# Kernel tuning notes

Measured on AMD Instinct MI355X. Metric: run time of the kernel, lower is better.

## Reference

```python
import jax, jax.numpy as jnp
import numpy as np

N = 1_000_000          # number of query points
POINT_DIMS = 2         # (x, y) coordinates
NUM_EMB = 6572         # number of video frames
EMB_DIM = 32
HIDDEN = 128


def setup_inputs() -> dict:
    key = jax.random.key(0)
    ks = jax.random.split(key, 10)
    x = jax.random.uniform(ks[0], (N, POINT_DIMS), dtype=jnp.float32)
    # fractional frame index in [0, NUM_EMB - 1)
    embeddings = jax.random.uniform(ks[1], (N,), dtype=jnp.float32) * (NUM_EMB - 1)
    em_table = jax.random.normal(ks[2], (NUM_EMB, EMB_DIM), dtype=jnp.float32) * 0.1
    in0 = POINT_DIMS + EMB_DIM
    W0 = jax.random.normal(ks[3], (in0, HIDDEN), dtype=jnp.float32) / np.sqrt(in0)
    b0 = jax.random.normal(ks[4], (HIDDEN,), dtype=jnp.float32) * 0.01
    W1 = jax.random.normal(ks[5], (HIDDEN, HIDDEN), dtype=jnp.float32) / np.sqrt(HIDDEN)
    b1 = jax.random.normal(ks[6], (HIDDEN,), dtype=jnp.float32) * 0.01
    W2 = jax.random.normal(ks[7], (HIDDEN, 1), dtype=jnp.float32) / np.sqrt(HIDDEN)
    b2 = jax.random.normal(ks[8], (1,), dtype=jnp.float32) * 0.01
    return {"x": x, "embeddings": embeddings, "em_table": em_table,
            "W0": W0, "b0": b0, "W1": W1, "b1": b1, "W2": W2, "b2": b2}


def reference(x, embeddings, em_table, W0, b0, W1, b1, W2, b2):
    num_emb = em_table.shape[0]
    em1 = embeddings.astype(jnp.int32)                       # floor (inputs >= 0)
    em2 = jnp.minimum(em1 + 1, num_emb - 1)                  # clamp(em1+1, max=E-1)
    res = (embeddings - em1.astype(jnp.float32))[:, None]    # [N, 1]
    e1 = em_table[em1]                                       # [N, 32] gather
    e2 = em_table[em2]                                       # [N, 32] gather
    em = e1 + (e2 - e1) * res                                # lerp
    h = jnp.concatenate((x, em), axis=1) @ W0 + b0           # [N, 128]
    h = jnp.clip(h, 0.0, 1.0)
    h = jnp.clip(h @ W1 + b1, 0.0, 1.0)
    out = jax.nn.sigmoid(h @ W2 + b2)                        # [N, 1]
    return out
```

## Files before the change

### kernel.cpp

```cpp
#include <hip/hip_runtime.h>
#include <hip/hip_bf16.h>


using bf16x8 = __attribute__((ext_vector_type(8))) short;
using f32x4  = __attribute__((ext_vector_type(4))) float;

#define NPTS    1000000
#define NUMEMB  6572
#define HID     128
#define M_IT    64
#define A0S     72
#define H0S     136
#define TILES   (NPTS / M_IT)
#define NBLOCKS 768

__device__ __forceinline__ unsigned short bf16r(float f) {
    unsigned u;
    __builtin_memcpy(&u, &f, 4);
    u = (u + 0x7fffu + ((u >> 16) & 1u)) >> 16;
    return (unsigned short)u;
}
__device__ __forceinline__ unsigned pk2(float a, float b) {
    float2 f2; f2.x = a; f2.y = b;
    __hip_bfloat162 h = __float22bfloat162_rn(f2);
    unsigned u;
    __builtin_memcpy(&u, &h, 4);
    return u;
}
__device__ __forceinline__ float clamp01(float x) {
    return __builtin_amdgcn_fmed3f(x, 0.f, 1.f);
}

__global__ __launch_bounds__(256, 3)
void mlp_fused(const float* __restrict__ x,
               const float* __restrict__ emb,
               const float* __restrict__ em_table,
               const float* __restrict__ W0, const float* __restrict__ b0,
               const float* __restrict__ W1, const float* __restrict__ b1,
               const float* __restrict__ W2, const float* __restrict__ b2,
               float* __restrict__ out)
{
    __shared__ __align__(16) unsigned short A0[2 * M_IT * A0S];
    __shared__ __align__(16) unsigned short H0[M_IT * H0S];
    __shared__ __align__(16) float PART[16][65];

    const int tid  = threadIdx.x;
    const int lane = tid & 63;
    const int nq   = tid >> 6;
    const int q    = lane >> 4;
    const int cl   = lane & 15;
    const int p    = tid >> 2;
    const int s    = tid & 3;

    for (int i = tid; i < 2 * M_IT * A0S; i += 256) A0[i] = 0;

    const int hcol = nq * 32 + (cl >> 2) * 8 + (cl & 3);
    bf16x8 w0t[2][2];
    for (int hb = 0; hb < 2; ++hb)
        for (int kt = 0; kt < 2; ++kt) {
            const int col = hcol + hb * 4;
            bf16x8 v;
            #pragma unroll
            for (int e = 0; e < 8; ++e) {
                const int k = kt * 32 + q * 8 + e;
                float val = 0.f;
                if (k < 32)       val = W0[(2 + k) * HID + col];
                else if (k == 32) val = W0[0 * HID + col];
                else if (k == 33) val = W0[1 * HID + col];
                v[e] = (short)bf16r(val);
            }
            w0t[hb][kt] = v;
        }

    bf16x8 w1r[2][4];
    for (int hb = 0; hb < 2; ++hb)
        for (int kk = 0; kk < 4; ++kk) {
            const int kt  = (nq + kk) & 3;
            const int col = hcol + hb * 4;
            bf16x8 v;
            #pragma unroll
            for (int e = 0; e < 8; ++e) {
                const int k = kt * 32 + q * 8 + e;
                v[e] = (short)bf16r(W1[k * HID + col]);
            }
            w1r[hb][kk] = v;
        }

    f32x4 b0q[2], b1q[2], w2q[2];
    for (int hb = 0; hb < 2; ++hb)
        for (int r = 0; r < 4; ++r) {
            const int h = nq * 32 + q * 8 + hb * 4 + r;
            b0q[hb][r] = b0[h];
            b1q[hb][r] = b1[h];
            w2q[hb][r] = W2[h];
        }
    const float bias2 = b2[0];

    int t = blockIdx.x;
    int cur = 0;
    {
        const int gp = t * M_IT + p;
        const float fe = emb[gp];
        float2 xv = {0.f, 0.f};
        if (s == 0) xv = *(const float2*)(x + 2 * gp);
        const int e1 = (int)fe;
        const int e2 = (e1 + 1 < NUMEMB) ? e1 + 1 : NUMEMB - 1;
        const float r = fe - (float)e1;
        const float4* p1 = (const float4*)(em_table + e1 * 32 + s * 8);
        const float4* p2 = (const float4*)(em_table + e2 * 32 + s * 8);
        const float4 g0 = p1[0], g1 = p1[1], g2 = p2[0], g3 = p2[1];
        uint4 d;
        d.x = pk2(g0.x + (g2.x - g0.x) * r, g0.y + (g2.y - g0.y) * r);
        d.y = pk2(g0.z + (g2.z - g0.z) * r, g0.w + (g2.w - g0.w) * r);
        d.z = pk2(g1.x + (g3.x - g1.x) * r, g1.y + (g3.y - g1.y) * r);
        d.w = pk2(g1.z + (g3.z - g1.z) * r, g1.w + (g3.w - g1.w) * r);
        *(uint4*)&A0[p * A0S + s * 8] = d;
        if (s == 0) *(unsigned*)&A0[p * A0S + 32] = pk2(xv.x, xv.y);
    }
    float  feB;
    float2 xvB = {0.f, 0.f};
    {
        int t1 = t + gridDim.x; if (t1 >= TILES) t1 = t;
        const int gp = t1 * M_IT + p;
        feB = emb[gp];
        if (s == 0) xvB = *(const float2*)(x + 2 * gp);
    }

    __syncthreads();

    for (; t < TILES; t += gridDim.x, cur ^= 1) {
        const int base = t * M_IT;
        const unsigned short* A0c = A0 + cur * (M_IT * A0S);
        unsigned short*       A0n = A0 + (cur ^ 1) * (M_IT * A0S);

        f32x4 acc[4][2];
        #pragma unroll
        for (int pb = 0; pb < 4; ++pb)
            #pragma unroll
            for (int hb = 0; hb < 2; ++hb)
                acc[pb][hb] = b0q[hb];
        #pragma unroll
        for (int pb = 0; pb < 4; ++pb) {
            #pragma unroll
            for (int kt = 0; kt < 2; ++kt) {
                bf16x8 bfrag = *(const bf16x8*)
                    &A0c[(pb * 16 + cl) * A0S + kt * 32 + q * 8];
                #pragma unroll
                for (int hb = 0; hb < 2; ++hb)
                    acc[pb][hb] = __builtin_amdgcn_mfma_f32_16x16x32_bf16(
                        w0t[hb][kt], bfrag, acc[pb][hb], 0, 0, 0);
            }
        }

        const int ge1 = (int)feB;
        const int ge2 = (ge1 + 1 < NUMEMB) ? ge1 + 1 : NUMEMB - 1;
        const float4* gp1 = (const float4*)(em_table + ge1 * 32 + s * 8);
        const float4* gp2 = (const float4*)(em_table + ge2 * 32 + s * 8);
        const float4 g0 = gp1[0], g1 = gp1[1], g2 = gp2[0], g3 = gp2[1];

        uint4 own[4];
        #pragma unroll
        for (int pb = 0; pb < 4; ++pb) {
            const f32x4 v0 = acc[pb][0], v1 = acc[pb][1];
            uint4 w;
            w.x = pk2(clamp01(v0[0]), clamp01(v0[1]));
            w.y = pk2(clamp01(v0[2]), clamp01(v0[3]));
            w.z = pk2(clamp01(v1[0]), clamp01(v1[1]));
            w.w = pk2(clamp01(v1[2]), clamp01(v1[3]));
            own[pb] = w;
            *(uint4*)&H0[(pb * 16 + cl) * H0S + nq * 32 + q * 8] = w;
        }

        {
            const float r = feB - (float)ge1;
            uint4 d;
            d.x = pk2(g0.x + (g2.x - g0.x) * r, g0.y + (g2.y - g0.y) * r);
            d.y = pk2(g0.z + (g2.z - g0.z) * r, g0.w + (g2.w - g0.w) * r);
            d.z = pk2(g1.x + (g3.x - g1.x) * r, g1.y + (g3.y - g1.y) * r);
            d.w = pk2(g1.z + (g3.z - g1.z) * r, g1.w + (g3.w - g1.w) * r);
            *(uint4*)&A0n[p * A0S + s * 8] = d;
            if (s == 0) *(unsigned*)&A0n[p * A0S + 32] = pk2(xvB.x, xvB.y);
        }
        {
            int t2 = t + 2 * (int)gridDim.x; if (t2 >= TILES) t2 = t;
            const int gp = t2 * M_IT + p;
            feB = emb[gp];
            if (s == 0) xvB = *(const float2*)(x + 2 * gp);
        }
        __syncthreads();

        #pragma unroll
        for (int pb = 0; pb < 4; ++pb)
            #pragma unroll
            for (int hb = 0; hb < 2; ++hb)
                acc[pb][hb] = b1q[hb];
        #pragma unroll
        for (int pb = 0; pb < 4; ++pb) {
            bf16x8 bfrag;
            __builtin_memcpy(&bfrag, &own[pb], 16);
            #pragma unroll
            for (int hb = 0; hb < 2; ++hb)
                acc[pb][hb] = __builtin_amdgcn_mfma_f32_16x16x32_bf16(
                    w1r[hb][0], bfrag, acc[pb][hb], 0, 0, 0);
        }
        #pragma unroll
        for (int kk = 1; kk < 4; ++kk) {
            const int kcol = (((nq + kk) & 3) << 5) + q * 8;
            #pragma unroll
            for (int pb = 0; pb < 4; ++pb) {
                bf16x8 bfrag = *(const bf16x8*)
                    &H0[(pb * 16 + cl) * H0S + kcol];
                #pragma unroll
                for (int hb = 0; hb < 2; ++hb)
                    acc[pb][hb] = __builtin_amdgcn_mfma_f32_16x16x32_bf16(
                        w1r[hb][kk], bfrag, acc[pb][hb], 0, 0, 0);
            }
        }

        #pragma unroll
        for (int pb = 0; pb < 4; ++pb) {
            float sum = 0.f;
            #pragma unroll
            for (int hb = 0; hb < 2; ++hb) {
                const f32x4 v = acc[pb][hb];
                sum += clamp01(v[0]) * w2q[hb][0];
                sum += clamp01(v[1]) * w2q[hb][1];
                sum += clamp01(v[2]) * w2q[hb][2];
                sum += clamp01(v[3]) * w2q[hb][3];
            }
            PART[nq * 4 + q][pb * 16 + cl] = sum;
        }
        __syncthreads();

        if (tid < 64) {
            float z = bias2;
            #pragma unroll
            for (int i = 0; i < 16; ++i) z += PART[i][tid];
            out[base + tid] = 1.f / (1.f + __expf(-z));
        }
    }
}

extern "C" void kernel_launch(void* const* d_in, const int* in_sizes, int n_in,
                              void* d_out, int out_size, void* d_ws, size_t ws_size,
                              hipStream_t stream) {
    const float* x   = (const float*)d_in[0];
    const float* emb = (const float*)d_in[1];
    const float* emt = (const float*)d_in[2];
    const float* W0  = (const float*)d_in[3];
    const float* b0  = (const float*)d_in[4];
    const float* W1  = (const float*)d_in[5];
    const float* b1  = (const float*)d_in[6];
    const float* W2  = (const float*)d_in[7];
    const float* b2  = (const float*)d_in[8];
    mlp_fused<<<NBLOCKS, 256, 0, stream>>>(x, emb, emt, W0, b0, W1, b1, W2, b2,
                                           (float*)d_out);
}
```

Before: 126.5 us.

## Split MFMA work 2x2 across waves to cut LDS reads of hidden layer

Each wave now owns 64 hidden columns for 32 points instead of 32 columns for all 64 points. Two of the four K-slices of layer 1 then come from the wave's own registers rather than LDS, which halves the H0 reads and the partial-sum reduction. The cost is twice the weight-fragment registers per wave. To fit them, launch bounds drop to 2 blocks per CU and the grid shrinks to 512 blocks, which lowers occupancy and latency hiding for the embedding gathers.

```diff
diff --git a/kernel.cpp b/kernel.cpp
--- a/kernel.cpp
+++ b/kernel.cpp
@@ -12,7 +12,7 @@
 #define A0S     72
 #define H0S     136
 #define TILES   (NPTS / M_IT)
-#define NBLOCKS 768
+#define NBLOCKS 512
 
 __device__ __forceinline__ unsigned short bf16r(float f) {
     unsigned u;
@@ -31,7 +31,7 @@
     return __builtin_amdgcn_fmed3f(x, 0.f, 1.f);
 }
 
-__global__ __launch_bounds__(256, 3)
+__global__ __launch_bounds__(256, 2)
 void mlp_fused(const float* __restrict__ x,
                const float* __restrict__ emb,
                const float* __restrict__ em_table,
@@ -42,23 +42,26 @@
 {
     __shared__ __align__(16) unsigned short A0[2 * M_IT * A0S];
     __shared__ __align__(16) unsigned short H0[M_IT * H0S];
-    __shared__ __align__(16) float PART[16][65];
+    __shared__ __align__(16) float PART2[8][65];
 
     const int tid  = threadIdx.x;
     const int lane = tid & 63;
-    const int nq   = tid >> 6;
+    const int w    = tid >> 6;
+    const int h2   = w & 1;
+    const int p2   = w >> 1;
     const int q    = lane >> 4;
     const int cl   = lane & 15;
     const int p    = tid >> 2;
     const int s    = tid & 3;
+    const int pbase = p2 * 32;
 
     for (int i = tid; i < 2 * M_IT * A0S; i += 256) A0[i] = 0;
 
-    const int hcol = nq * 32 + (cl >> 2) * 8 + (cl & 3);
-    bf16x8 w0t[2][2];
-    for (int hb = 0; hb < 2; ++hb)
+    const int mrow = (cl >> 2) * 8 + (cl & 3);
+    bf16x8 w0t[4][2];
+    for (int hb = 0; hb < 4; ++hb)
         for (int kt = 0; kt < 2; ++kt) {
-            const int col = hcol + hb * 4;
+            const int col = h2 * 64 + (hb >> 1) * 32 + mrow + (hb & 1) * 4;
             bf16x8 v;
             #pragma unroll
             for (int e = 0; e < 8; ++e) {
@@ -72,24 +75,24 @@
             w0t[hb][kt] = v;
         }
 
-    bf16x8 w1r[2][4];
-    for (int hb = 0; hb < 2; ++hb)
+    bf16x8 w1r[4][4];
+    for (int hb = 0; hb < 4; ++hb)
         for (int kk = 0; kk < 4; ++kk) {
-            const int kt  = (nq + kk) & 3;
-            const int col = hcol + hb * 4;
+            const int ktg = (h2 * 2 + kk) & 3;
+            const int col = h2 * 64 + (hb >> 1) * 32 + mrow + (hb & 1) * 4;
             bf16x8 v;
             #pragma unroll
             for (int e = 0; e < 8; ++e) {
-                const int k = kt * 32 + q * 8 + e;
+                const int k = ktg * 32 + q * 8 + e;
                 v[e] = (short)bf16r(W1[k * HID + col]);
             }
             w1r[hb][kk] = v;
         }
 
-    f32x4 b0q[2], b1q[2], w2q[2];
-    for (int hb = 0; hb < 2; ++hb)
+    f32x4 b0q[4], b1q[4], w2q[4];
+    for (int hb = 0; hb < 4; ++hb)
         for (int r = 0; r < 4; ++r) {
-            const int h = nq * 32 + q * 8 + hb * 4 + r;
+            const int h = h2 * 64 + (hb >> 1) * 32 + q * 8 + (hb & 1) * 4 + r;
             b0q[hb][r] = b0[h];
             b1q[hb][r] = b1[h];
             w2q[hb][r] = W2[h];
@@ -107,8 +110,8 @@
         const int e2 = (e1 + 1 < NUMEMB) ? e1 + 1 : NUMEMB - 1;
         const float r = fe - (float)e1;
         const float4* p1 = (const float4*)(em_table + e1 * 32 + s * 8);
-        const float4* p2 = (const float4*)(em_table + e2 * 32 + s * 8);
-        const float4 g0 = p1[0], g1 = p1[1], g2 = p2[0], g3 = p2[1];
+        const float4* p2p = (const float4*)(em_table + e2 * 32 + s * 8);
+        const float4 g0 = p1[0], g1 = p1[1], g2 = p2p[0], g3 = p2p[1];
         uint4 d;
         d.x = pk2(g0.x + (g2.x - g0.x) * r, g0.y + (g2.y - g0.y) * r);
         d.y = pk2(g0.z + (g2.z - g0.z) * r, g0.w + (g2.w - g0.w) * r);
@@ -133,20 +136,20 @@
         const unsigned short* A0c = A0 + cur * (M_IT * A0S);
         unsigned short*       A0n = A0 + (cur ^ 1) * (M_IT * A0S);
 
-        f32x4 acc[4][2];
-        #pragma unroll
-        for (int pb = 0; pb < 4; ++pb)
-            #pragma unroll
-            for (int hb = 0; hb < 2; ++hb)
+        f32x4 acc[2][4];
+        #pragma unroll
+        for (int pb = 0; pb < 2; ++pb)
+            #pragma unroll
+            for (int hb = 0; hb < 4; ++hb)
                 acc[pb][hb] = b0q[hb];
         #pragma unroll
-        for (int pb = 0; pb < 4; ++pb) {
+        for (int pb = 0; pb < 2; ++pb) {
             #pragma unroll
             for (int kt = 0; kt < 2; ++kt) {
                 bf16x8 bfrag = *(const bf16x8*)
-                    &A0c[(pb * 16 + cl) * A0S + kt * 32 + q * 8];
+                    &A0c[(pbase + pb * 16 + cl) * A0S + kt * 32 + q * 8];
                 #pragma unroll
-                for (int hb = 0; hb < 2; ++hb)
+                for (int hb = 0; hb < 4; ++hb)
                     acc[pb][hb] = __builtin_amdgcn_mfma_f32_16x16x32_bf16(
                         w0t[hb][kt], bfrag, acc[pb][hb], 0, 0, 0);
             }
@@ -158,18 +161,22 @@
         const float4* gp2 = (const float4*)(em_table + ge2 * 32 + s * 8);
         const float4 g0 = gp1[0], g1 = gp1[1], g2 = gp2[0], g3 = gp2[1];
 
-        uint4 own[4];
-        #pragma unroll
-        for (int pb = 0; pb < 4; ++pb) {
-            const f32x4 v0 = acc[pb][0], v1 = acc[pb][1];
-            uint4 w;
-            w.x = pk2(clamp01(v0[0]), clamp01(v0[1]));
-            w.y = pk2(clamp01(v0[2]), clamp01(v0[3]));
-            w.z = pk2(clamp01(v1[0]), clamp01(v1[1]));
-            w.w = pk2(clamp01(v1[2]), clamp01(v1[3]));
-            own[pb] = w;
-            *(uint4*)&H0[(pb * 16 + cl) * H0S + nq * 32 + q * 8] = w;
-        }
+        uint4 own[2][2];
+        #pragma unroll
+        for (int pb = 0; pb < 2; ++pb)
+            #pragma unroll
+            for (int ktl = 0; ktl < 2; ++ktl) {
+                const f32x4 v0 = acc[pb][2 * ktl + 0];
+                const f32x4 v1 = acc[pb][2 * ktl + 1];
+                uint4 wv;
+                wv.x = pk2(clamp01(v0[0]), clamp01(v0[1]));
+                wv.y = pk2(clamp01(v0[2]), clamp01(v0[3]));
+                wv.z = pk2(clamp01(v1[0]), clamp01(v1[1]));
+                wv.w = pk2(clamp01(v1[2]), clamp01(v1[3]));
+                own[pb][ktl] = wv;
+                *(uint4*)&H0[(pbase + pb * 16 + cl) * H0S
+                             + h2 * 64 + ktl * 32 + q * 8] = wv;
+            }
 
         {
             const float r = feB - (float)ge1;
@@ -190,52 +197,55 @@
         __syncthreads();
 
         #pragma unroll
-        for (int pb = 0; pb < 4; ++pb)
-            #pragma unroll
-            for (int hb = 0; hb < 2; ++hb)
+        for (int pb = 0; pb < 2; ++pb)
+            #pragma unroll
+            for (int hb = 0; hb < 4; ++hb)
                 acc[pb][hb] = b1q[hb];
         #pragma unroll
-        for (int pb = 0; pb < 4; ++pb) {
-            bf16x8 bfrag;
-            __builtin_memcpy(&bfrag, &own[pb], 16);
-            #pragma unroll
-            for (int hb = 0; hb < 2; ++hb)
-                acc[pb][hb] = __builtin_amdgcn_mfma_f32_16x16x32_bf16(
-                    w1r[hb][0], bfrag, acc[pb][hb], 0, 0, 0);
-        }
-        #pragma unroll
-        for (int kk = 1; kk < 4; ++kk) {
-            const int kcol = (((nq + kk) & 3) << 5) + q * 8;
-            #pragma unroll
-            for (int pb = 0; pb < 4; ++pb) {
-                bf16x8 bfrag = *(const bf16x8*)
-                    &H0[(pb * 16 + cl) * H0S + kcol];
+        for (int kk = 0; kk < 2; ++kk) {
+            #pragma unroll
+            for (int pb = 0; pb < 2; ++pb) {
+                bf16x8 bfrag;
+                __builtin_memcpy(&bfrag, &own[pb][kk], 16);
                 #pragma unroll
-                for (int hb = 0; hb < 2; ++hb)
+                for (int hb = 0; hb < 4; ++hb)
                     acc[pb][hb] = __builtin_amdgcn_mfma_f32_16x16x32_bf16(
                         w1r[hb][kk], bfrag, acc[pb][hb], 0, 0, 0);
             }
         }
-
-        #pragma unroll
-        for (int pb = 0; pb < 4; ++pb) {
+        #pragma unroll
+        for (int kk = 2; kk < 4; ++kk) {
+            const int koff = (((h2 * 2 + kk) & 3) << 5) + q * 8;
+            #pragma unroll
+            for (int pb = 0; pb < 2; ++pb) {
+                bf16x8 bfrag = *(const bf16x8*)
+                    &H0[(pbase + pb * 16 + cl) * H0S + koff];
+                #pragma unroll
+                for (int hb = 0; hb < 4; ++hb)
+                    acc[pb][hb] = __builtin_amdgcn_mfma_f32_16x16x32_bf16(
+                        w1r[hb][kk], bfrag, acc[pb][hb], 0, 0, 0);
+            }
+        }
+
+        #pragma unroll
+        for (int pb = 0; pb < 2; ++pb) {
             float sum = 0.f;
             #pragma unroll
-            for (int hb = 0; hb < 2; ++hb) {
+            for (int hb = 0; hb < 4; ++hb) {
                 const f32x4 v = acc[pb][hb];
                 sum += clamp01(v[0]) * w2q[hb][0];
                 sum += clamp01(v[1]) * w2q[hb][1];
                 sum += clamp01(v[2]) * w2q[hb][2];
                 sum += clamp01(v[3]) * w2q[hb][3];
             }
-            PART[nq * 4 + q][pb * 16 + cl] = sum;
+            PART2[h2 * 4 + q][pbase + pb * 16 + cl] = sum;
         }
         __syncthreads();
 
         if (tid < 64) {
             float z = bias2;
             #pragma unroll
-            for (int i = 0; i < 16; ++i) z += PART[i][tid];
+            for (int i = 0; i < 8; ++i) z += PART2[i][tid];
             out[base + tid] = 1.f / (1.f + __expf(-z));
         }
     }
```

After: 132.9 us. 1.05x slower.
